# Optimization experiments

Measured on AMD Instinct MI355X. Metric: run time of the kernel, lower is better.

The kernel has to match this reference:

```python
import jax, jax.numpy as jnp
import numpy as np

EMBED = 768
HEAD = 128

def setup_inputs() -> dict:
    key = jax.random.key(0)
    ks = jax.random.split(key, 8)
    B, S = 8, 2048
    x = jax.random.normal(ks[0], (B, S, EMBED), dtype=jnp.float32)
    enc_output = jax.random.normal(ks[1], (B, S, EMBED), dtype=jnp.float32)
    s = 1.0 / np.sqrt(EMBED)
    Wq = jax.random.normal(ks[2], (EMBED, HEAD), dtype=jnp.float32) * s
    Wk = jax.random.normal(ks[3], (EMBED, HEAD), dtype=jnp.float32) * s
    Wv = jax.random.normal(ks[4], (EMBED, HEAD), dtype=jnp.float32) * s
    bq = jnp.zeros((HEAD,), dtype=jnp.float32)
    bk = jnp.zeros((HEAD,), dtype=jnp.float32)
    bv = jnp.zeros((HEAD,), dtype=jnp.float32)
    return {"x": x, "enc_output": enc_output, "Wq": Wq, "bq": bq,
            "Wk": Wk, "bk": bk, "Wv": Wv, "bv": bv}

def reference(x, enc_output, Wq, bq, Wk, bk, Wv, bv):
    # Faithful to original: Q, K, V all from x (enc_output is unused in the
    # original forward); scale is embed_size ** 0.5; dropout never applied.
    q = jnp.einsum('nse,ed->nsd', x, Wq) + bq  # [B,S,H]
    k = jnp.einsum('nse,ed->nsd', x, Wk) + bk
    v = jnp.einsum('nse,ed->nsd', x, Wv) + bv
    energy = jnp.einsum('nqd,nkd->nqk', q, k)  # [B,S,S]
    attn = jax.nn.softmax(energy / jnp.sqrt(jnp.float32(EMBED)), axis=2)
    out = jnp.einsum('nql,nld->nqd', attn, v)  # [B,S,H]
    return out
```

## Files before the change

### kernel.cpp

```cpp
#include <hip/hip_runtime.h>
#include <hip/hip_bf16.h>


typedef __bf16 bf16x8 __attribute__((ext_vector_type(8)));
typedef float f32x4 __attribute__((ext_vector_type(4)));
using bf16 = __hip_bfloat16;

#define EMB 768
#define HD 128
#define SEQ 2048
#define BATCH 8
#define ROWS (BATCH * SEQ)
#define NSPLIT 4
#define TILES_PER_SPLIT (SEQ / 64 / NSPLIT)

__device__ inline void cvt_store8(bf16* dst, float4 a, float4 b) {
    union { bf16 h[8]; uint4 u; } t;
    t.h[0] = __float2bfloat16(a.x); t.h[1] = __float2bfloat16(a.y);
    t.h[2] = __float2bfloat16(a.z); t.h[3] = __float2bfloat16(a.w);
    t.h[4] = __float2bfloat16(b.x); t.h[5] = __float2bfloat16(b.y);
    t.h[6] = __float2bfloat16(b.z); t.h[7] = __float2bfloat16(b.w);
    *reinterpret_cast<uint4*>(dst) = t.u;
}

__global__ __launch_bounds__(256) void wt_kernel(
    const float* __restrict__ Wq, const float* __restrict__ Wk,
    const float* __restrict__ Wv, bf16* __restrict__ Wt)
{
    __shared__ float t_lds[32][33];
    const int tid = threadIdx.x;
    const int k0 = blockIdx.x * 32;
    const int n0 = blockIdx.y * 32;
    const int mtx = blockIdx.z;
    const float* W = (mtx == 0) ? Wq : (mtx == 1) ? Wk : Wv;
    const int j = tid & 31, i0 = tid >> 5;
#pragma unroll
    for (int c = 0; c < 4; ++c)
        t_lds[i0 + 8 * c][j] = W[(size_t)(k0 + i0 + 8 * c) * HD + n0 + j];
    __syncthreads();
#pragma unroll
    for (int c = 0; c < 4; ++c)
        Wt[(size_t)mtx * HD * EMB + (size_t)(n0 + i0 + 8 * c) * EMB + k0 + j] =
            __float2bfloat16(t_lds[j][i0 + 8 * c]);
}

__global__ __launch_bounds__(256) void qkv_kernel(
    const float* __restrict__ x, const bf16* __restrict__ Wt,
    const float* __restrict__ bq, const float* __restrict__ bk,
    const float* __restrict__ bv,
    bf16* __restrict__ Q, bf16* __restrict__ K, bf16* __restrict__ Vt)
{
    __shared__ alignas(16) bf16 a_lds[64][68];
    __shared__ alignas(16) bf16 b_lds[128][68];
    const int tid  = threadIdx.x;
    const int sel  = blockIdx.y;
    const int row0 = blockIdx.x * 64;
    const bf16* Wsel = Wt + (size_t)sel * HD * EMB;
    const int lane = tid & 63, wave = tid >> 6;
    const int lr = lane & 15, lq = lane >> 4;

    f32x4 acc[8];
#pragma unroll
    for (int j = 0; j < 8; ++j) acc[j] = f32x4{0.f, 0.f, 0.f, 0.f};

    for (int kt = 0; kt < EMB / 64; ++kt) {
#pragma unroll
        for (int c = 0; c < 2; ++c) {
            int lin = tid + c * 256;
            int r = lin >> 3, ch = lin & 7;
            const float* src = &x[(size_t)(row0 + r) * EMB + kt * 64 + ch * 8];
            float4 f0 = *reinterpret_cast<const float4*>(src);
            float4 f1 = *reinterpret_cast<const float4*>(src + 4);
            cvt_store8(&a_lds[r][ch * 8], f0, f1);
        }
#pragma unroll
        for (int c = 0; c < 4; ++c) {
            int lin = tid + c * 256;
            int r = lin >> 3, ch = lin & 7;
            *reinterpret_cast<uint4*>(&b_lds[r][ch * 8]) =
                *reinterpret_cast<const uint4*>(&Wsel[(size_t)r * EMB + kt * 64 + ch * 8]);
        }
        __syncthreads();
#pragma unroll
        for (int ks = 0; ks < 2; ++ks) {
            bf16x8 a = *reinterpret_cast<const bf16x8*>(&a_lds[wave * 16 + lr][ks * 32 + lq * 8]);
#pragma unroll
            for (int nt = 0; nt < 8; ++nt) {
                bf16x8 b = *reinterpret_cast<const bf16x8*>(&b_lds[nt * 16 + lr][ks * 32 + lq * 8]);
                acc[nt] = __builtin_amdgcn_mfma_f32_16x16x32_bf16(a, b, acc[nt], 0, 0, 0);
            }
        }
        __syncthreads();
    }

    bf16 (*o_lds)[132] = reinterpret_cast<bf16(*)[132]>(&b_lds[0][0]);
    const float* bias = (sel == 0) ? bq : (sel == 1) ? bk : bv;
#pragma unroll
    for (int nt = 0; nt < 8; ++nt) {
        int col = nt * 16 + lr;
        float bb = bias[col];
#pragma unroll
        for (int rg = 0; rg < 4; ++rg)
            o_lds[wave * 16 + lq * 4 + rg][col] = __float2bfloat16(acc[nt][rg] + bb);
    }
    __syncthreads();
    if (sel < 2) {
        bf16* dst = (sel == 0) ? Q : K;
#pragma unroll
        for (int c = 0; c < 4; ++c) {
            int lin = tid + c * 256;
            int r = lin >> 4, ch = lin & 15;
            *reinterpret_cast<uint4*>(&dst[(size_t)(row0 + r) * HD + ch * 8]) =
                *reinterpret_cast<const uint4*>(&o_lds[r][ch * 8]);
        }
    } else {
        int d = tid >> 1, sh = (tid & 1) * 32;
        int bi = row0 >> 11, s0 = row0 & (SEQ - 1);
        union { bf16 h[32]; uint4 u4[4]; } pk;
#pragma unroll
        for (int s = 0; s < 32; ++s) pk.h[s] = o_lds[sh + s][d];
        bf16* base = &Vt[((size_t)bi * HD + d) * SEQ + s0 + sh];
#pragma unroll
        for (int c = 0; c < 4; ++c)
            *reinterpret_cast<uint4*>(base + c * 8) = pk.u4[c];
    }
}

__global__ __launch_bounds__(256) void flash_kernel(
    const bf16* __restrict__ Q, const bf16* __restrict__ K,
    const bf16* __restrict__ Vt,
    float* __restrict__ Opart, float* __restrict__ Lpart)
{
    __shared__ alignas(16) bf16 k_lds[64][132];
    __shared__ alignas(16) bf16 v_lds[144][68];
    __shared__ alignas(16) bf16 p_lds[4][16][72];
    const int tid = threadIdx.x;
    const int lane = tid & 63, wave = tid >> 6;
    const int lr = lane & 15, lq = lane >> 4;
    const int b  = blockIdx.y;
    const int split = blockIdx.z;
    const int q0 = blockIdx.x * 64;
    const int qrow = b * SEQ + q0 + wave * 16;

    const float sc = 0.03608439182435161f * 1.44269504088896f;

    for (int i = tid; i < 16 * 68; i += 256) {
        int r = i / 68, c = i % 68;
        v_lds[128 + r][c] = __float2bfloat16(r == 0 ? 1.0f : 0.0f);
    }

    bf16x8 qf[4];
#pragma unroll
    for (int ks = 0; ks < 4; ++ks)
        qf[ks] = *reinterpret_cast<const bf16x8*>(&Q[(size_t)(qrow + lr) * HD + ks * 32 + lq * 8]);

    f32x4 o[9];
#pragma unroll
    for (int d = 0; d < 9; ++d) o[d] = f32x4{0.f, 0.f, 0.f, 0.f};

    for (int t = split * TILES_PER_SPLIT; t < (split + 1) * TILES_PER_SPLIT; ++t) {
        __syncthreads();
#pragma unroll
        for (int c = 0; c < 4; ++c) {
            int lin = tid + c * 256;
            int r = lin >> 4, ch = lin & 15;
            *reinterpret_cast<uint4*>(&k_lds[r][ch * 8]) =
                *reinterpret_cast<const uint4*>(&K[(size_t)(b * SEQ + t * 64 + r) * HD + ch * 8]);
        }
#pragma unroll
        for (int c = 0; c < 4; ++c) {
            int lin = tid + c * 256;
            int r = lin >> 3, ch = lin & 7;
            *reinterpret_cast<uint4*>(&v_lds[r][ch * 8]) =
                *reinterpret_cast<const uint4*>(&Vt[((size_t)b * HD + r) * SEQ + t * 64 + ch * 8]);
        }
        __syncthreads();

        f32x4 s[4];
#pragma unroll
        for (int nt = 0; nt < 4; ++nt) {
            s[nt] = f32x4{0.f, 0.f, 0.f, 0.f};
#pragma unroll
            for (int ks = 0; ks < 4; ++ks) {
                bf16x8 kf = *reinterpret_cast<const bf16x8*>(&k_lds[nt * 16 + lr][ks * 32 + lq * 8]);
                s[nt] = __builtin_amdgcn_mfma_f32_16x16x32_bf16(kf, qf[ks], s[nt], 0, 0, 0);
            }
        }

#pragma unroll
        for (int nt = 0; nt < 4; ++nt) {
            union { bf16 h[4]; uint2 u; } pk;
#pragma unroll
            for (int r = 0; r < 4; ++r)
                pk.h[r] = __float2bfloat16(exp2f(__builtin_fmaf(s[nt][r], sc, -8.0f)));
            *reinterpret_cast<uint2*>(&p_lds[wave][lr][nt * 16 + lq * 4]) = pk.u;
        }

#pragma unroll
        for (int ks = 0; ks < 2; ++ks) {
            bf16x8 pf = *reinterpret_cast<const bf16x8*>(&p_lds[wave][lr][ks * 32 + lq * 8]);
#pragma unroll
            for (int d = 0; d < 9; ++d) {
                bf16x8 vf = *reinterpret_cast<const bf16x8*>(&v_lds[d * 16 + lr][ks * 32 + lq * 8]);
                o[d] = __builtin_amdgcn_mfma_f32_16x16x32_bf16(vf, pf, o[d], 0, 0, 0);
            }
        }
    }

    const size_t obase = (size_t)split * ROWS;
#pragma unroll
    for (int d = 0; d < 8; ++d)
        *reinterpret_cast<f32x4*>(&Opart[(obase + qrow + lr) * HD + d * 16 + lq * 4]) = o[d];
    if (lane < 16)
        Lpart[obase + qrow + lr] = o[8][0];
}

__global__ __launch_bounds__(256) void combine_kernel(
    const float* __restrict__ Opart, const float* __restrict__ Lpart,
    float* __restrict__ out)
{
    int gid = blockIdx.x * 256 + threadIdx.x;
    int row = gid >> 5, dc = gid & 31;
    float L = 0.f;
#pragma unroll
    for (int s = 0; s < NSPLIT; ++s)
        L += Lpart[(size_t)s * ROWS + row];
    float4 acc = {0.f, 0.f, 0.f, 0.f};
#pragma unroll
    for (int s = 0; s < NSPLIT; ++s) {
        float4 v = *reinterpret_cast<const float4*>(&Opart[((size_t)s * ROWS + row) * HD + dc * 4]);
        acc.x += v.x; acc.y += v.y; acc.z += v.z; acc.w += v.w;
    }
    float inv = 1.f / L;
    acc.x *= inv; acc.y *= inv; acc.z *= inv; acc.w *= inv;
    *reinterpret_cast<float4*>(&out[(size_t)row * HD + dc * 4]) = acc;
}

extern "C" void kernel_launch(void* const* d_in, const int* in_sizes, int n_in,
                              void* d_out, int out_size, void* d_ws, size_t ws_size,
                              hipStream_t stream) {
    const float* x  = (const float*)d_in[0];
    const float* Wq = (const float*)d_in[2];
    const float* bq = (const float*)d_in[3];
    const float* Wk = (const float*)d_in[4];
    const float* bk = (const float*)d_in[5];
    const float* Wv = (const float*)d_in[6];
    const float* bv = (const float*)d_in[7];
    float* out = (float*)d_out;

    char* ws = (char*)d_ws;
    const size_t WT_BYTES  = (size_t)3 * HD * EMB * 2;
    const size_t QKV_BYTES = (size_t)ROWS * HD * 2;
    const size_t OP_BYTES  = (size_t)NSPLIT * ROWS * HD * 4;
    bf16*  Wt    = (bf16*)ws;
    bf16*  Qb    = (bf16*)(ws + WT_BYTES);
    bf16*  Kb    = (bf16*)(ws + WT_BYTES + QKV_BYTES);
    bf16*  Vt    = (bf16*)(ws + WT_BYTES + 2 * QKV_BYTES);
    float* Opart = (float*)(ws + WT_BYTES + 3 * QKV_BYTES);
    float* Lpart = (float*)(ws + WT_BYTES + 3 * QKV_BYTES + OP_BYTES);

    hipLaunchKernelGGL(wt_kernel, dim3(EMB / 32, HD / 32, 3), dim3(256), 0, stream,
                       Wq, Wk, Wv, Wt);
    hipLaunchKernelGGL(qkv_kernel, dim3(ROWS / 64, 3), dim3(256), 0, stream,
                       x, Wt, bq, bk, bv, Qb, Kb, Vt);
    hipLaunchKernelGGL(flash_kernel, dim3(SEQ / 64, BATCH, NSPLIT), dim3(256), 0, stream,
                       Qb, Kb, Vt, Opart, Lpart);
    hipLaunchKernelGGL(combine_kernel, dim3(ROWS * 32 / 256), dim3(256), 0, stream,
                       Opart, Lpart, out);
}
```

Before: 203.3 us.

## Prefetch next tiles into registers in QKV projection and attention loops

```diff
diff --git a/kernel.cpp b/kernel.cpp
--- a/kernel.cpp
+++ b/kernel.cpp
@@ -50,8 +50,8 @@
     const float* __restrict__ bv,
     bf16* __restrict__ Q, bf16* __restrict__ K, bf16* __restrict__ Vt)
 {
-    __shared__ alignas(16) bf16 a_lds[64][68];
-    __shared__ alignas(16) bf16 b_lds[128][68];
+    __shared__ alignas(16) bf16 a_lds[2][64][68];
+    __shared__ alignas(16) bf16 b_lds[2][128][68];
     const int tid  = threadIdx.x;
     const int sel  = blockIdx.y;
     const int row0 = blockIdx.x * 64;
@@ -59,41 +59,68 @@
     const int lane = tid & 63, wave = tid >> 6;
     const int lr = lane & 15, lq = lane >> 4;
 
+    float4 fa[2][2];
+    uint4  fb[4];
+
+    auto load_regs = [&](int kt) {
+#pragma unroll
+        for (int c = 0; c < 2; ++c) {
+            int lin = tid + c * 256;
+            int r = lin >> 3, ch = lin & 7;
+            const float* src = &x[(size_t)(row0 + r) * EMB + kt * 64 + ch * 8];
+            fa[c][0] = *reinterpret_cast<const float4*>(src);
+            fa[c][1] = *reinterpret_cast<const float4*>(src + 4);
+        }
+#pragma unroll
+        for (int c = 0; c < 4; ++c) {
+            int lin = tid + c * 256;
+            int r = lin >> 3, ch = lin & 7;
+            fb[c] = *reinterpret_cast<const uint4*>(&Wsel[(size_t)r * EMB + kt * 64 + ch * 8]);
+        }
+    };
+    auto store_lds = [&](int buf) {
+#pragma unroll
+        for (int c = 0; c < 2; ++c) {
+            int lin = tid + c * 256;
+            int r = lin >> 3, ch = lin & 7;
+            cvt_store8(&a_lds[buf][r][ch * 8], fa[c][0], fa[c][1]);
+        }
+#pragma unroll
+        for (int c = 0; c < 4; ++c) {
+            int lin = tid + c * 256;
+            int r = lin >> 3, ch = lin & 7;
+            *reinterpret_cast<uint4*>(&b_lds[buf][r][ch * 8]) = fb[c];
+        }
+    };
+
     f32x4 acc[8];
 #pragma unroll
     for (int j = 0; j < 8; ++j) acc[j] = f32x4{0.f, 0.f, 0.f, 0.f};
 
+    load_regs(0);
+    store_lds(0);
+    __syncthreads();
+
     for (int kt = 0; kt < EMB / 64; ++kt) {
-#pragma unroll
-        for (int c = 0; c < 2; ++c) {
-            int lin = tid + c * 256;
-            int r = lin >> 3, ch = lin & 7;
-            const float* src = &x[(size_t)(row0 + r) * EMB + kt * 64 + ch * 8];
-            float4 f0 = *reinterpret_cast<const float4*>(src);
-            float4 f1 = *reinterpret_cast<const float4*>(src + 4);
-            cvt_store8(&a_lds[r][ch * 8], f0, f1);
-        }
-#pragma unroll
-        for (int c = 0; c < 4; ++c) {
-            int lin = tid + c * 256;
-            int r = lin >> 3, ch = lin & 7;
-            *reinterpret_cast<uint4*>(&b_lds[r][ch * 8]) =
-                *reinterpret_cast<const uint4*>(&Wsel[(size_t)r * EMB + kt * 64 + ch * 8]);
-        }
-        __syncthreads();
+        const int cur = kt & 1;
+        if (kt < EMB / 64 - 1) load_regs(kt + 1);
 #pragma unroll
         for (int ks = 0; ks < 2; ++ks) {
-            bf16x8 a = *reinterpret_cast<const bf16x8*>(&a_lds[wave * 16 + lr][ks * 32 + lq * 8]);
+            bf16x8 a = *reinterpret_cast<const bf16x8*>(&a_lds[cur][wave * 16 + lr][ks * 32 + lq * 8]);
 #pragma unroll
             for (int nt = 0; nt < 8; ++nt) {
-                bf16x8 b = *reinterpret_cast<const bf16x8*>(&b_lds[nt * 16 + lr][ks * 32 + lq * 8]);
+                bf16x8 b = *reinterpret_cast<const bf16x8*>(&b_lds[cur][nt * 16 + lr][ks * 32 + lq * 8]);
                 acc[nt] = __builtin_amdgcn_mfma_f32_16x16x32_bf16(a, b, acc[nt], 0, 0, 0);
             }
         }
-        __syncthreads();
-    }
-
-    bf16 (*o_lds)[132] = reinterpret_cast<bf16(*)[132]>(&b_lds[0][0]);
+        if (kt < EMB / 64 - 1) {
+            __syncthreads();
+            store_lds(1 - cur);
+            __syncthreads();
+        }
+    }
+
+    bf16 (*o_lds)[132] = reinterpret_cast<bf16(*)[132]>(&b_lds[0][0][0]);
     const float* bias = (sel == 0) ? bq : (sel == 1) ? bk : bv;
 #pragma unroll
     for (int nt = 0; nt < 8; ++nt) {
@@ -154,26 +181,44 @@
     for (int ks = 0; ks < 4; ++ks)
         qf[ks] = *reinterpret_cast<const bf16x8*>(&Q[(size_t)(qrow + lr) * HD + ks * 32 + lq * 8]);
 
+    uint4 rk[4], rv[4];
+    auto load_kv = [&](int t) {
+#pragma unroll
+        for (int c = 0; c < 4; ++c) {
+            int lin = tid + c * 256;
+            int r = lin >> 4, ch = lin & 15;
+            rk[c] = *reinterpret_cast<const uint4*>(&K[(size_t)(b * SEQ + t * 64 + r) * HD + ch * 8]);
+        }
+#pragma unroll
+        for (int c = 0; c < 4; ++c) {
+            int lin = tid + c * 256;
+            int r = lin >> 3, ch = lin & 7;
+            rv[c] = *reinterpret_cast<const uint4*>(&Vt[((size_t)b * HD + r) * SEQ + t * 64 + ch * 8]);
+        }
+    };
+
     f32x4 o[9];
 #pragma unroll
     for (int d = 0; d < 9; ++d) o[d] = f32x4{0.f, 0.f, 0.f, 0.f};
 
-    for (int t = split * TILES_PER_SPLIT; t < (split + 1) * TILES_PER_SPLIT; ++t) {
+    load_kv(split * TILES_PER_SPLIT);
+
+    for (int i = 0; i < TILES_PER_SPLIT; ++i) {
         __syncthreads();
 #pragma unroll
         for (int c = 0; c < 4; ++c) {
             int lin = tid + c * 256;
             int r = lin >> 4, ch = lin & 15;
-            *reinterpret_cast<uint4*>(&k_lds[r][ch * 8]) =
-                *reinterpret_cast<const uint4*>(&K[(size_t)(b * SEQ + t * 64 + r) * HD + ch * 8]);
-        }
-#pragma unroll
-        for (int c = 0; c < 4; ++c) {
-            int lin = tid + c * 256;
-            int r = lin >> 3, ch = lin & 7;
-            *reinterpret_cast<uint4*>(&v_lds[r][ch * 8]) =
-                *reinterpret_cast<const uint4*>(&Vt[((size_t)b * HD + r) * SEQ + t * 64 + ch * 8]);
-        }
+            *reinterpret_cast<uint4*>(&k_lds[r][ch * 8]) = rk[c];
+        }
+#pragma unroll
+        for (int c = 0; c < 4; ++c) {
+            int lin = tid + c * 256;
+            int r = lin >> 3, ch = lin & 7;
+            *reinterpret_cast<uint4*>(&v_lds[r][ch * 8]) = rv[c];
+        }
+        if (i + 1 < TILES_PER_SPLIT)
+            load_kv(split * TILES_PER_SPLIT + i + 1);
         __syncthreads();
 
         f32x4 s[4];
```

Measured after the change: 276.0 us. 1.36x slower.

## Restructure flash kernel wave split and shrink QKV projection tiles

Applied to the files above, without the earlier changes.

```diff
diff --git a/kernel.cpp b/kernel.cpp
--- a/kernel.cpp
+++ b/kernel.cpp
@@ -50,24 +50,24 @@
     const float* __restrict__ bv,
     bf16* __restrict__ Q, bf16* __restrict__ K, bf16* __restrict__ Vt)
 {
-    __shared__ alignas(16) bf16 a_lds[64][68];
-    __shared__ alignas(16) bf16 b_lds[128][68];
+    __shared__ alignas(16) bf16 a_lds[32][72];
+    __shared__ alignas(16) bf16 b_lds[128][72];
     const int tid  = threadIdx.x;
     const int sel  = blockIdx.y;
-    const int row0 = blockIdx.x * 64;
+    const int row0 = blockIdx.x * 32;
     const bf16* Wsel = Wt + (size_t)sel * HD * EMB;
     const int lane = tid & 63, wave = tid >> 6;
     const int lr = lane & 15, lq = lane >> 4;
-
-    f32x4 acc[8];
-#pragma unroll
-    for (int j = 0; j < 8; ++j) acc[j] = f32x4{0.f, 0.f, 0.f, 0.f};
+    const int mstrip = (wave & 1) * 16;
+    const int nhalf  = (wave >> 1) * 64;
+
+    f32x4 acc[4];
+#pragma unroll
+    for (int j = 0; j < 4; ++j) acc[j] = f32x4{0.f, 0.f, 0.f, 0.f};
 
     for (int kt = 0; kt < EMB / 64; ++kt) {
-#pragma unroll
-        for (int c = 0; c < 2; ++c) {
-            int lin = tid + c * 256;
-            int r = lin >> 3, ch = lin & 7;
+        {
+            int r = tid >> 3, ch = tid & 7;
             const float* src = &x[(size_t)(row0 + r) * EMB + kt * 64 + ch * 8];
             float4 f0 = *reinterpret_cast<const float4*>(src);
             float4 f1 = *reinterpret_cast<const float4*>(src + 4);
@@ -83,10 +83,10 @@
         __syncthreads();
 #pragma unroll
         for (int ks = 0; ks < 2; ++ks) {
-            bf16x8 a = *reinterpret_cast<const bf16x8*>(&a_lds[wave * 16 + lr][ks * 32 + lq * 8]);
-#pragma unroll
-            for (int nt = 0; nt < 8; ++nt) {
-                bf16x8 b = *reinterpret_cast<const bf16x8*>(&b_lds[nt * 16 + lr][ks * 32 + lq * 8]);
+            bf16x8 a = *reinterpret_cast<const bf16x8*>(&a_lds[mstrip + lr][ks * 32 + lq * 8]);
+#pragma unroll
+            for (int nt = 0; nt < 4; ++nt) {
+                bf16x8 b = *reinterpret_cast<const bf16x8*>(&b_lds[nhalf + nt * 16 + lr][ks * 32 + lq * 8]);
                 acc[nt] = __builtin_amdgcn_mfma_f32_16x16x32_bf16(a, b, acc[nt], 0, 0, 0);
             }
         }
@@ -96,123 +96,142 @@
     bf16 (*o_lds)[132] = reinterpret_cast<bf16(*)[132]>(&b_lds[0][0]);
     const float* bias = (sel == 0) ? bq : (sel == 1) ? bk : bv;
 #pragma unroll
-    for (int nt = 0; nt < 8; ++nt) {
-        int col = nt * 16 + lr;
+    for (int nt = 0; nt < 4; ++nt) {
+        int col = nhalf + nt * 16 + lr;
         float bb = bias[col];
 #pragma unroll
         for (int rg = 0; rg < 4; ++rg)
-            o_lds[wave * 16 + lq * 4 + rg][col] = __float2bfloat16(acc[nt][rg] + bb);
+            o_lds[mstrip + lq * 4 + rg][col] = __float2bfloat16(acc[nt][rg] + bb);
     }
     __syncthreads();
     if (sel < 2) {
         bf16* dst = (sel == 0) ? Q : K;
-#pragma unroll
-        for (int c = 0; c < 4; ++c) {
-            int lin = tid + c * 256;
-            int r = lin >> 4, ch = lin & 15;
-            *reinterpret_cast<uint4*>(&dst[(size_t)(row0 + r) * HD + ch * 8]) =
-                *reinterpret_cast<const uint4*>(&o_lds[r][ch * 8]);
-        }
+        int r = tid >> 3, ch = (tid & 7) * 16;
+        *reinterpret_cast<uint4*>(&dst[(size_t)(row0 + r) * HD + ch]) =
+            *reinterpret_cast<const uint4*>(&o_lds[r][ch]);
+        *reinterpret_cast<uint4*>(&dst[(size_t)(row0 + r) * HD + ch + 8]) =
+            *reinterpret_cast<const uint4*>(&o_lds[r][ch + 8]);
     } else {
-        int d = tid >> 1, sh = (tid & 1) * 32;
+        int d = tid >> 1, sh = (tid & 1) * 16;
         int bi = row0 >> 11, s0 = row0 & (SEQ - 1);
-        union { bf16 h[32]; uint4 u4[4]; } pk;
-#pragma unroll
-        for (int s = 0; s < 32; ++s) pk.h[s] = o_lds[sh + s][d];
+        union { bf16 h[16]; uint4 u4[2]; } pk;
+#pragma unroll
+        for (int s = 0; s < 16; ++s) pk.h[s] = o_lds[sh + s][d];
         bf16* base = &Vt[((size_t)bi * HD + d) * SEQ + s0 + sh];
-#pragma unroll
-        for (int c = 0; c < 4; ++c)
-            *reinterpret_cast<uint4*>(base + c * 8) = pk.u4[c];
-    }
-}
-
-__global__ __launch_bounds__(256) void flash_kernel(
+        *reinterpret_cast<uint4*>(base)     = pk.u4[0];
+        *reinterpret_cast<uint4*>(base + 8) = pk.u4[1];
+    }
+}
+
+__global__ __launch_bounds__(256, 4) void flash_kernel(
     const bf16* __restrict__ Q, const bf16* __restrict__ K,
     const bf16* __restrict__ Vt,
     float* __restrict__ Opart, float* __restrict__ Lpart)
 {
-    __shared__ alignas(16) bf16 k_lds[64][132];
-    __shared__ alignas(16) bf16 v_lds[144][68];
-    __shared__ alignas(16) bf16 p_lds[4][16][72];
+    __shared__ alignas(16) bf16 v_lds[128][72];
+    __shared__ alignas(16) bf16 p_lds[64][72];
     const int tid = threadIdx.x;
     const int lane = tid & 63, wave = tid >> 6;
     const int lr = lane & 15, lq = lane >> 4;
     const int b  = blockIdx.y;
     const int split = blockIdx.z;
     const int q0 = blockIdx.x * 64;
-    const int qrow = b * SEQ + q0 + wave * 16;
+    const int qbase = b * SEQ + q0;
 
     const float sc = 0.03608439182435161f * 1.44269504088896f;
 
-    for (int i = tid; i < 16 * 68; i += 256) {
-        int r = i / 68, c = i % 68;
-        v_lds[128 + r][c] = __float2bfloat16(r == 0 ? 1.0f : 0.0f);
-    }
-
-    bf16x8 qf[4];
-#pragma unroll
-    for (int ks = 0; ks < 4; ++ks)
-        qf[ks] = *reinterpret_cast<const bf16x8*>(&Q[(size_t)(qrow + lr) * HD + ks * 32 + lq * 8]);
-
-    f32x4 o[9];
-#pragma unroll
-    for (int d = 0; d < 9; ++d) o[d] = f32x4{0.f, 0.f, 0.f, 0.f};
-
-    for (int t = split * TILES_PER_SPLIT; t < (split + 1) * TILES_PER_SPLIT; ++t) {
-        __syncthreads();
-#pragma unroll
-        for (int c = 0; c < 4; ++c) {
-            int lin = tid + c * 256;
-            int r = lin >> 4, ch = lin & 15;
-            *reinterpret_cast<uint4*>(&k_lds[r][ch * 8]) =
-                *reinterpret_cast<const uint4*>(&K[(size_t)(b * SEQ + t * 64 + r) * HD + ch * 8]);
-        }
+    f32x4 o[2][4];
+#pragma unroll
+    for (int dt = 0; dt < 2; ++dt)
+#pragma unroll
+        for (int qt = 0; qt < 4; ++qt) o[dt][qt] = f32x4{0.f, 0.f, 0.f, 0.f};
+    float lsum[4] = {0.f, 0.f, 0.f, 0.f};
+
+    for (int i = 0; i < TILES_PER_SPLIT; ++i) {
+        const int t = split * TILES_PER_SPLIT + i;
+        uint4 rv[4];
 #pragma unroll
         for (int c = 0; c < 4; ++c) {
             int lin = tid + c * 256;
             int r = lin >> 3, ch = lin & 7;
-            *reinterpret_cast<uint4*>(&v_lds[r][ch * 8]) =
-                *reinterpret_cast<const uint4*>(&Vt[((size_t)b * HD + r) * SEQ + t * 64 + ch * 8]);
-        }
-        __syncthreads();
-
-        f32x4 s[4];
-#pragma unroll
-        for (int nt = 0; nt < 4; ++nt) {
-            s[nt] = f32x4{0.f, 0.f, 0.f, 0.f};
+            rv[c] = *reinterpret_cast<const uint4*>(&Vt[((size_t)b * HD + r) * SEQ + t * 64 + ch * 8]);
+        }
+        bf16x8 kf[4];
+#pragma unroll
+        for (int ks = 0; ks < 4; ++ks)
+            kf[ks] = *reinterpret_cast<const bf16x8*>(
+                &K[(size_t)(b * SEQ + t * 64 + wave * 16 + lr) * HD + ks * 32 + lq * 8]);
+
+#pragma unroll
+        for (int qt = 0; qt < 4; ++qt) {
+            f32x4 s = f32x4{0.f, 0.f, 0.f, 0.f};
 #pragma unroll
             for (int ks = 0; ks < 4; ++ks) {
-                bf16x8 kf = *reinterpret_cast<const bf16x8*>(&k_lds[nt * 16 + lr][ks * 32 + lq * 8]);
-                s[nt] = __builtin_amdgcn_mfma_f32_16x16x32_bf16(kf, qf[ks], s[nt], 0, 0, 0);
-            }
-        }
-
-#pragma unroll
-        for (int nt = 0; nt < 4; ++nt) {
+                bf16x8 qf = *reinterpret_cast<const bf16x8*>(
+                    &Q[(size_t)(qbase + qt * 16 + lr) * HD + ks * 32 + lq * 8]);
+                s = __builtin_amdgcn_mfma_f32_16x16x32_bf16(kf[ks], qf, s, 0, 0, 0);
+            }
             union { bf16 h[4]; uint2 u; } pk;
-#pragma unroll
-            for (int r = 0; r < 4; ++r)
-                pk.h[r] = __float2bfloat16(exp2f(__builtin_fmaf(s[nt][r], sc, -8.0f)));
-            *reinterpret_cast<uint2*>(&p_lds[wave][lr][nt * 16 + lq * 4]) = pk.u;
-        }
+            float rs = 0.f;
+#pragma unroll
+            for (int r = 0; r < 4; ++r) {
+                bf16 pv = __float2bfloat16(exp2f(__builtin_fmaf(s[r], sc, -8.0f)));
+                pk.h[r] = pv;
+                rs += __bfloat162float(pv);
+            }
+            lsum[qt] += rs;
+            *reinterpret_cast<uint2*>(&p_lds[qt * 16 + lr][wave * 16 + lq * 4]) = pk.u;
+        }
+
+#pragma unroll
+        for (int c = 0; c < 4; ++c) {
+            int lin = tid + c * 256;
+            int r = lin >> 3, ch = lin & 7;
+            *reinterpret_cast<uint4*>(&v_lds[r][ch * 8]) = rv[c];
+        }
+        __syncthreads();
 
 #pragma unroll
         for (int ks = 0; ks < 2; ++ks) {
-            bf16x8 pf = *reinterpret_cast<const bf16x8*>(&p_lds[wave][lr][ks * 32 + lq * 8]);
-#pragma unroll
-            for (int d = 0; d < 9; ++d) {
-                bf16x8 vf = *reinterpret_cast<const bf16x8*>(&v_lds[d * 16 + lr][ks * 32 + lq * 8]);
-                o[d] = __builtin_amdgcn_mfma_f32_16x16x32_bf16(vf, pf, o[d], 0, 0, 0);
-            }
-        }
+#pragma unroll
+            for (int dt = 0; dt < 2; ++dt) {
+                bf16x8 vf = *reinterpret_cast<const bf16x8*>(
+                    &v_lds[wave * 32 + dt * 16 + lr][ks * 32 + lq * 8]);
+#pragma unroll
+                for (int qt = 0; qt < 4; ++qt) {
+                    bf16x8 pf = *reinterpret_cast<const bf16x8*>(
+                        &p_lds[qt * 16 + lr][ks * 32 + lq * 8]);
+                    o[dt][qt] = __builtin_amdgcn_mfma_f32_16x16x32_bf16(vf, pf, o[dt][qt], 0, 0, 0);
+                }
+            }
+        }
+        __syncthreads();
     }
 
     const size_t obase = (size_t)split * ROWS;
 #pragma unroll
-    for (int d = 0; d < 8; ++d)
-        *reinterpret_cast<f32x4*>(&Opart[(obase + qrow + lr) * HD + d * 16 + lq * 4]) = o[d];
-    if (lane < 16)
-        Lpart[obase + qrow + lr] = o[8][0];
+    for (int dt = 0; dt < 2; ++dt)
+#pragma unroll
+        for (int qt = 0; qt < 4; ++qt)
+            *reinterpret_cast<f32x4*>(
+                &Opart[(obase + qbase + qt * 16 + lr) * HD + wave * 32 + dt * 16 + lq * 4]) = o[dt][qt];
+
+#pragma unroll
+    for (int qt = 0; qt < 4; ++qt) {
+        lsum[qt] += __shfl_xor(lsum[qt], 16);
+        lsum[qt] += __shfl_xor(lsum[qt], 32);
+    }
+    float* red = reinterpret_cast<float*>(&p_lds[0][0]);
+    if (lq == 0) {
+#pragma unroll
+        for (int qt = 0; qt < 4; ++qt)
+            red[wave * 64 + qt * 16 + lr] = lsum[qt];
+    }
+    __syncthreads();
+    if (wave == 0) {
+        float L = red[lane] + red[64 + lane] + red[128 + lane] + red[192 + lane];
+        Lpart[obase + qbase + lane] = L;
+    }
 }
 
 __global__ __launch_bounds__(256) void combine_kernel(
@@ -261,7 +280,7 @@
 
     hipLaunchKernelGGL(wt_kernel, dim3(EMB / 32, HD / 32, 3), dim3(256), 0, stream,
                        Wq, Wk, Wv, Wt);
-    hipLaunchKernelGGL(qkv_kernel, dim3(ROWS / 64, 3), dim3(256), 0, stream,
+    hipLaunchKernelGGL(qkv_kernel, dim3(ROWS / 32, 3), dim3(256), 0, stream,
                        x, Wt, bq, bk, bv, Qb, Kb, Vt);
     hipLaunchKernelGGL(flash_kernel, dim3(SEQ / 64, BATCH, NSPLIT), dim3(256), 0, stream,
                        Qb, Kb, Vt, Opart, Lpart);
```

New measurement: 229.3 us. +12.8%, slower.

## Process two 16-row query tiles per wave to reuse K and V fragments

Applied to the files above, without the earlier changes.

```diff
diff --git a/kernel.cpp b/kernel.cpp
--- a/kernel.cpp
+++ b/kernel.cpp
@@ -126,21 +126,21 @@
     }
 }
 
-__global__ __launch_bounds__(256) void flash_kernel(
+__global__ __launch_bounds__(256, 2) void flash_kernel(
     const bf16* __restrict__ Q, const bf16* __restrict__ K,
     const bf16* __restrict__ Vt,
     float* __restrict__ Opart, float* __restrict__ Lpart)
 {
     __shared__ alignas(16) bf16 k_lds[64][132];
     __shared__ alignas(16) bf16 v_lds[144][68];
-    __shared__ alignas(16) bf16 p_lds[4][16][72];
+    __shared__ alignas(16) bf16 p_lds[4][32][72];
     const int tid = threadIdx.x;
     const int lane = tid & 63, wave = tid >> 6;
     const int lr = lane & 15, lq = lane >> 4;
     const int b  = blockIdx.y;
     const int split = blockIdx.z;
-    const int q0 = blockIdx.x * 64;
-    const int qrow = b * SEQ + q0 + wave * 16;
+    const int q0 = blockIdx.x * 128;
+    const int qrow = b * SEQ + q0 + wave * 32;
 
     const float sc = 0.03608439182435161f * 1.44269504088896f;
 
@@ -149,14 +149,19 @@
         v_lds[128 + r][c] = __float2bfloat16(r == 0 ? 1.0f : 0.0f);
     }
 
-    bf16x8 qf[4];
-#pragma unroll
-    for (int ks = 0; ks < 4; ++ks)
-        qf[ks] = *reinterpret_cast<const bf16x8*>(&Q[(size_t)(qrow + lr) * HD + ks * 32 + lq * 8]);
-
-    f32x4 o[9];
-#pragma unroll
-    for (int d = 0; d < 9; ++d) o[d] = f32x4{0.f, 0.f, 0.f, 0.f};
+    bf16x8 qf[2][4];
+#pragma unroll
+    for (int qt = 0; qt < 2; ++qt)
+#pragma unroll
+        for (int ks = 0; ks < 4; ++ks)
+            qf[qt][ks] = *reinterpret_cast<const bf16x8*>(
+                &Q[(size_t)(qrow + qt * 16 + lr) * HD + ks * 32 + lq * 8]);
+
+    f32x4 o[2][9];
+#pragma unroll
+    for (int qt = 0; qt < 2; ++qt)
+#pragma unroll
+        for (int d = 0; d < 9; ++d) o[qt][d] = f32x4{0.f, 0.f, 0.f, 0.f};
 
     for (int t = split * TILES_PER_SPLIT; t < (split + 1) * TILES_PER_SPLIT; ++t) {
         __syncthreads();
@@ -176,43 +181,53 @@
         }
         __syncthreads();
 
-        f32x4 s[4];
 #pragma unroll
         for (int nt = 0; nt < 4; ++nt) {
-            s[nt] = f32x4{0.f, 0.f, 0.f, 0.f};
-#pragma unroll
-            for (int ks = 0; ks < 4; ++ks) {
-                bf16x8 kf = *reinterpret_cast<const bf16x8*>(&k_lds[nt * 16 + lr][ks * 32 + lq * 8]);
-                s[nt] = __builtin_amdgcn_mfma_f32_16x16x32_bf16(kf, qf[ks], s[nt], 0, 0, 0);
+            bf16x8 kf[4];
+#pragma unroll
+            for (int ks = 0; ks < 4; ++ks)
+                kf[ks] = *reinterpret_cast<const bf16x8*>(&k_lds[nt * 16 + lr][ks * 32 + lq * 8]);
+#pragma unroll
+            for (int qt = 0; qt < 2; ++qt) {
+                f32x4 s = f32x4{0.f, 0.f, 0.f, 0.f};
+#pragma unroll
+                for (int ks = 0; ks < 4; ++ks)
+                    s = __builtin_amdgcn_mfma_f32_16x16x32_bf16(kf[ks], qf[qt][ks], s, 0, 0, 0);
+                union { bf16 h[4]; uint2 u; } pk;
+#pragma unroll
+                for (int r = 0; r < 4; ++r)
+                    pk.h[r] = __float2bfloat16(exp2f(__builtin_fmaf(s[r], sc, -8.0f)));
+                *reinterpret_cast<uint2*>(&p_lds[wave][qt * 16 + lr][nt * 16 + lq * 4]) = pk.u;
             }
         }
 
 #pragma unroll
-        for (int nt = 0; nt < 4; ++nt) {
-            union { bf16 h[4]; uint2 u; } pk;
-#pragma unroll
-            for (int r = 0; r < 4; ++r)
-                pk.h[r] = __float2bfloat16(exp2f(__builtin_fmaf(s[nt][r], sc, -8.0f)));
-            *reinterpret_cast<uint2*>(&p_lds[wave][lr][nt * 16 + lq * 4]) = pk.u;
-        }
-
-#pragma unroll
         for (int ks = 0; ks < 2; ++ks) {
-            bf16x8 pf = *reinterpret_cast<const bf16x8*>(&p_lds[wave][lr][ks * 32 + lq * 8]);
+            bf16x8 pf[2];
+#pragma unroll
+            for (int qt = 0; qt < 2; ++qt)
+                pf[qt] = *reinterpret_cast<const bf16x8*>(
+                    &p_lds[wave][qt * 16 + lr][ks * 32 + lq * 8]);
 #pragma unroll
             for (int d = 0; d < 9; ++d) {
                 bf16x8 vf = *reinterpret_cast<const bf16x8*>(&v_lds[d * 16 + lr][ks * 32 + lq * 8]);
-                o[d] = __builtin_amdgcn_mfma_f32_16x16x32_bf16(vf, pf, o[d], 0, 0, 0);
+#pragma unroll
+                for (int qt = 0; qt < 2; ++qt)
+                    o[qt][d] = __builtin_amdgcn_mfma_f32_16x16x32_bf16(vf, pf[qt], o[qt][d], 0, 0, 0);
             }
         }
     }
 
     const size_t obase = (size_t)split * ROWS;
 #pragma unroll
-    for (int d = 0; d < 8; ++d)
-        *reinterpret_cast<f32x4*>(&Opart[(obase + qrow + lr) * HD + d * 16 + lq * 4]) = o[d];
-    if (lane < 16)
-        Lpart[obase + qrow + lr] = o[8][0];
+    for (int qt = 0; qt < 2; ++qt) {
+#pragma unroll
+        for (int d = 0; d < 8; ++d)
+            *reinterpret_cast<f32x4*>(
+                &Opart[(obase + qrow + qt * 16 + lr) * HD + d * 16 + lq * 4]) = o[qt][d];
+        if (lane < 16)
+            Lpart[obase + qrow + qt * 16 + lr] = o[qt][8][0];
+    }
 }
 
 __global__ __launch_bounds__(256) void combine_kernel(
@@ -263,7 +278,7 @@
                        Wq, Wk, Wv, Wt);
     hipLaunchKernelGGL(qkv_kernel, dim3(ROWS / 64, 3), dim3(256), 0, stream,
                        x, Wt, bq, bk, bv, Qb, Kb, Vt);
-    hipLaunchKernelGGL(flash_kernel, dim3(SEQ / 64, BATCH, NSPLIT), dim3(256), 0, stream,
+    hipLaunchKernelGGL(flash_kernel, dim3(SEQ / 128, BATCH, NSPLIT), dim3(256), 0, stream,
                        Qb, Kb, Vt, Opart, Lpart);
     hipLaunchKernelGGL(combine_kernel, dim3(ROWS * 32 / 256), dim3(256), 0, stream,
                        Opart, Lpart, out);
```

After: 194.0 us. 4.6% less time.
